# Performance work log

Measured on AMD Instinct MI355X. Metric: run time of the kernel, lower is better.

Reference implementation:

```python
import jax, jax.numpy as jnp
import numpy as np

B, L, IN_DIM, OUT_DIM = 4, 2048, 64, 2
D_MODEL, N_LAYERS = 768, 4
D_STATE, EXPAND, D_CONV = 16, 2, 4
D_INNER = EXPAND * D_MODEL          # 1536
DT_RANK = -(-D_MODEL // 16)          # ceil(768/16) = 48
EPS = 1e-5


def rmsnorm(x, w):
    return x * jax.lax.rsqrt(jnp.mean(x * x, axis=-1, keepdims=True) + EPS) * w


def setup_inputs() -> dict:
    key = jax.random.key(0)
    ks = jax.random.split(key, 10)
    s = 0.02
    f = lambda k, shp: jax.random.normal(k, shp, jnp.float32) * s
    return dict(
        x=jax.random.normal(ks[0], (B, L, IN_DIM), jnp.float32),
        W1=f(ks[1], (D_MODEL, IN_DIM)),
        b1=jnp.zeros((D_MODEL,), jnp.float32),
        norm_w=jnp.ones((N_LAYERS, D_MODEL), jnp.float32),
        in_proj_w=f(ks[2], (N_LAYERS, 2 * D_INNER, D_MODEL)),
        conv_w=f(ks[3], (N_LAYERS, D_INNER, D_CONV)),
        conv_b=jnp.zeros((N_LAYERS, D_INNER), jnp.float32),
        x_proj_w=f(ks[4], (N_LAYERS, DT_RANK + 2 * D_STATE, D_INNER)),
        dt_proj_w=f(ks[5], (N_LAYERS, D_INNER, DT_RANK)),
        dt_proj_b=f(ks[6], (N_LAYERS, D_INNER)),
        A_log=jnp.log(jnp.broadcast_to(jnp.arange(1, D_STATE + 1, dtype=jnp.float32), (N_LAYERS, D_INNER, D_STATE))).copy(),
        D=jnp.ones((N_LAYERS, D_INNER), jnp.float32),
        out_proj_w=f(ks[7], (N_LAYERS, D_MODEL, D_INNER)),
        normf_w=jnp.ones((D_MODEL,), jnp.float32),
        W2=f(ks[8], (OUT_DIM, D_MODEL)),
        b2=jnp.zeros((OUT_DIM,), jnp.float32),
    )


def _block(h, p):
    # One Mamba residual block (mamba-minimal): h + out_proj(ssm(conv(in_proj(norm(h)))))
    norm_w, in_w, cw, cb, xp_w, dt_w, dt_b, A_log, Dp, out_w = p
    xn = rmsnorm(h, norm_w)
    xr = xn @ in_w.T                                  # [B,L,2*d_inner]
    xs, res = jnp.split(xr, 2, axis=-1)
    # causal depthwise conv1d, kernel D_CONV, left pad D_CONV-1
    xc = jax.lax.conv_general_dilated(
        xs.transpose(0, 2, 1), cw[:, None, :], (1,), [(D_CONV - 1, 0)],
        feature_group_count=D_INNER, dimension_numbers=('NCH', 'OIH', 'NCH'))
    xc = jax.nn.silu((xc + cb[None, :, None]).transpose(0, 2, 1))  # [B,L,d_inner]
    # selective SSM
    A = -jnp.exp(A_log)                               # [d_inner, n]
    dbl = xc @ xp_w.T                                 # [B,L,dt_rank+2n]
    dr = dbl[..., :DT_RANK]
    Bm = dbl[..., DT_RANK:DT_RANK + D_STATE]          # [B,L,n]
    Cm = dbl[..., DT_RANK + D_STATE:]                 # [B,L,n]
    delta = jax.nn.softplus(dr @ dt_w.T + dt_b)       # [B,L,d_inner]

    def step(s, t):
        d_t, B_t, C_t, u_t = t                        # [B,d_in],[B,n],[B,n],[B,d_in]
        dA = jnp.exp(d_t[..., None] * A)              # [B,d_in,n]
        s = dA * s + (d_t * u_t)[..., None] * B_t[:, None, :]
        y = jnp.einsum('bdn,bn->bd', s, C_t)
        return s, y

    init = jnp.zeros((h.shape[0], D_INNER, D_STATE), h.dtype)
    ts = (delta.transpose(1, 0, 2), Bm.transpose(1, 0, 2),
          Cm.transpose(1, 0, 2), xc.transpose(1, 0, 2))
    _, ys = jax.lax.scan(step, init, ts)
    y = ys.transpose(1, 0, 2) + xc * Dp               # [B,L,d_inner]
    y = y * jax.nn.silu(res)
    return h + y @ out_w.T


def _forward(x, W1, b1, norm_w, in_proj_w, conv_w, conv_b, x_proj_w,
             dt_proj_w, dt_proj_b, A_log, D, out_proj_w, normf_w, W2, b2):
    h = x @ W1.T + b1                                 # [B,L,d_model]
    params = (norm_w, in_proj_w, conv_w, conv_b, x_proj_w, dt_proj_w,
              dt_proj_b, A_log, D, out_proj_w)
    h, _ = jax.lax.scan(lambda c, p: (_block(c, p), None), h, params)
    h = rmsnorm(h, normf_w)
    logits = h @ W2.T + b2                            # [B,L,out_dim]
    probs = jax.nn.softmax(logits, axis=1)            # Softmax(dim=1) over L
    return probs.reshape(-1)                          # x.flatten()


def reference(x, W1, b1, norm_w, in_proj_w, conv_w, conv_b, x_proj_w,
              dt_proj_w, dt_proj_b, A_log, D, out_proj_w, normf_w, W2, b2):
    return _forward(x, W1, b1, norm_w, in_proj_w, conv_w, conv_b, x_proj_w,
                    dt_proj_w, dt_proj_b, A_log, D, out_proj_w, normf_w, W2, b2)
```

## Files before the change

kernel.cpp:

```cpp
#include <hip/hip_runtime.h>

typedef __bf16 bf16_t;
typedef bf16_t bf16x8 __attribute__((ext_vector_type(8)));
typedef float f32x4 __attribute__((ext_vector_type(4)));
typedef float f32x2 __attribute__((ext_vector_type(2)));

#define DEV_INLINE __device__ __forceinline__

#define BB 4
#define LL 2048
#define ROWS 8192
#define DMODEL 768
#define DINNER 1536
#define DIN2 3072
#define DTRANK 48
#define DSTATE 16

DEV_INLINE void glds16(const void* g, void* l) {
    __builtin_amdgcn_global_load_lds(
        (const __attribute__((address_space(1))) void*)(unsigned long long)g,
        (__attribute__((address_space(3))) void*)(unsigned int)(unsigned long long)l,
        16, 0, 0);
}

DEV_INLINE float bf2f(bf16_t v) { return (float)v; }
DEV_INLINE bf16_t f2bf(float v) { return (bf16_t)v; }

struct Ptrs { const void* p[16]; };

__device__ __constant__ const int g_off[16] = {
    0, 524288, 573440, 574208, 577280, 10014464, 10039040, 10045184,
    10536704, 10831616, 10837760, 10936064, 10942208, 15660800, 15661568, 15663104
};
__device__ __constant__ const int g_sz[16] = {
    524288, 49152, 768, 3072, 9437184, 24576, 6144, 491520,
    294912, 6144, 98304, 6144, 4718592, 768, 1536, 2
};
#define CONV_ELEMS 15663112

__global__ __launch_bounds__(256) void convert_inputs(Ptrs P, bf16_t* __restrict__ dst,
                                                      float* __restrict__ Aa)
{
    int gi = (blockIdx.x * 256 + threadIdx.x) * 8;
    if (gi >= CONV_ELEMS) return;
    bool isbf = (*(const unsigned*)P.p[3] == 0x3F803F80u);
    int seg = -1, rel = 0;
#pragma unroll
    for (int s = 0; s < 16; ++s) {
        int r = gi - g_off[s];
        if (r >= 0 && r < g_sz[s]) { seg = s; rel = r; }
    }
    if (seg >= 0 && rel + 8 <= g_sz[seg]) {
        const void* sp = P.p[seg];
        float f[8];
        if (isbf) {
            bf16x8 v = *(const bf16x8*)((const bf16_t*)sp + rel);
#pragma unroll
            for (int k = 0; k < 8; ++k) f[k] = bf2f(v[k]);
        } else {
            f32x4 v0 = *(const f32x4*)((const float*)sp + rel);
            f32x4 v1 = *(const f32x4*)((const float*)sp + rel + 4);
#pragma unroll
            for (int k = 0; k < 4; ++k) { f[k] = v0[k]; f[k + 4] = v1[k]; }
        }
        bf16x8 o;
#pragma unroll
        for (int k = 0; k < 8; ++k) o[k] = f2bf(f[k]);
        *(bf16x8*)(dst + gi) = o;
        if (seg == 10) {
#pragma unroll
            for (int k = 0; k < 8; ++k) Aa[rel + k] = -__expf(f[k]);
        }
    } else {
        for (int k = 0; k < 8; ++k) {
            int i = gi + k;
            int s2 = -1, r2 = 0;
#pragma unroll
            for (int s = 0; s < 16; ++s) {
                int r = i - g_off[s];
                if (r >= 0 && r < g_sz[s]) { s2 = s; r2 = r; }
            }
            if (s2 < 0) continue;
            const void* sp = P.p[s2];
            float fv = isbf ? bf2f(((const bf16_t*)sp)[r2]) : ((const float*)sp)[r2];
            dst[i] = f2bf(fv);
            if (s2 == 10) Aa[r2] = -__expf(fv);
        }
    }
}

__global__ __launch_bounds__(256) void gemm_bt128(
    const bf16_t* __restrict__ A, int lda,
    const bf16_t* __restrict__ W, int ldw,
    void* __restrict__ Cv, int ldc, int K,
    const bf16_t* __restrict__ bias, int epi)
{
    __shared__ bf16_t sA[2][128 * 32];
    __shared__ bf16_t sW[2][128 * 32];
    const int t = threadIdx.x;
    const int wv = t >> 6, lane = t & 63;
    const int qk = lane >> 4, lr = lane & 15;
    const int m0 = blockIdx.x * 128, n0 = blockIdx.y * 128;
    const int wm = (wv >> 1) * 64, wn = (wv & 1) * 64;

    int ch0 = (wv * 2 + 0) * 64 + lane;
    int ch1 = (wv * 2 + 1) * 64 + lane;
    int r0 = ch0 >> 2, g0 = (ch0 & 3) ^ ((r0 >> 1) & 3);
    int r1 = ch1 >> 2, g1 = (ch1 & 3) ^ ((r1 >> 1) & 3);

    f32x4 acc[4][4];
#pragma unroll
    for (int i = 0; i < 4; ++i)
#pragma unroll
        for (int j = 0; j < 4; ++j) acc[i][j] = (f32x4){0.f, 0.f, 0.f, 0.f};

    {
        glds16((const char*)(A + (size_t)(m0 + r0) * lda) + g0 * 16, (char*)sA[0] + ch0 * 16);
        glds16((const char*)(A + (size_t)(m0 + r1) * lda) + g1 * 16, (char*)sA[0] + ch1 * 16);
        glds16((const char*)(W + (size_t)(n0 + r0) * ldw) + g0 * 16, (char*)sW[0] + ch0 * 16);
        glds16((const char*)(W + (size_t)(n0 + r1) * ldw) + g1 * 16, (char*)sW[0] + ch1 * 16);
    }

    int nIter = K >> 5;
    for (int it = 0; it < nIter; ++it) {
        int cur = it & 1;
        __syncthreads();
        if (it + 1 < nIter) {
            int k1 = (it + 1) << 5;
            glds16((const char*)(A + (size_t)(m0 + r0) * lda + k1) + g0 * 16,
                   (char*)sA[1 - cur] + ch0 * 16);
            glds16((const char*)(A + (size_t)(m0 + r1) * lda + k1) + g1 * 16,
                   (char*)sA[1 - cur] + ch1 * 16);
            glds16((const char*)(W + (size_t)(n0 + r0) * ldw + k1) + g0 * 16,
                   (char*)sW[1 - cur] + ch0 * 16);
            glds16((const char*)(W + (size_t)(n0 + r1) * ldw + k1) + g1 * 16,
                   (char*)sW[1 - cur] + ch1 * 16);
        }

        bf16x8 af[4], wf[4];
#pragma unroll
        for (int i = 0; i < 4; ++i) {
            int row = wm + i * 16 + lr;
            int cc = qk ^ ((row >> 1) & 3);
            af[i] = *(const bf16x8*)((const char*)sA[cur] + row * 64 + cc * 16);
        }
#pragma unroll
        for (int j = 0; j < 4; ++j) {
            int row = wn + j * 16 + lr;
            int cc = qk ^ ((row >> 1) & 3);
            wf[j] = *(const bf16x8*)((const char*)sW[cur] + row * 64 + cc * 16);
        }
#pragma unroll
        for (int i = 0; i < 4; ++i)
#pragma unroll
            for (int j = 0; j < 4; ++j)
                acc[i][j] = __builtin_amdgcn_mfma_f32_16x16x32_bf16(af[i], wf[j], acc[i][j], 0, 0, 0);
    }

    float* Cf = (float*)Cv;
    bf16_t* Cb = (bf16_t*)Cv;
#pragma unroll
    for (int i = 0; i < 4; ++i) {
        int row = m0 + wm + i * 16 + qk * 4;
#pragma unroll
        for (int j = 0; j < 4; ++j) {
            int col = n0 + wn + j * 16 + lr;
#pragma unroll
            for (int r = 0; r < 4; ++r) {
                size_t idx = (size_t)(row + r) * ldc + col;
                float v = acc[i][j][r];
                if (epi == 1) v += bf2f(bias[col]);
                if (epi == 2) v += Cf[idx];
                if (epi == 3) Cb[idx] = f2bf(v);
                else Cf[idx] = v;
            }
        }
    }
}

__global__ __launch_bounds__(256) void gemm_outproj(
    const bf16_t* __restrict__ A,
    const bf16_t* __restrict__ W,
    float* __restrict__ Cf)
{
    __shared__ bf16_t sA[2][64 * 32];
    __shared__ bf16_t sW[2][128 * 32];
    const int t = threadIdx.x;
    const int wv = t >> 6, lane = t & 63;
    const int qk = lane >> 4, lr = lane & 15;
    const int m0 = blockIdx.x * 64, n0 = blockIdx.y * 128;
    const int wm = (wv >> 1) * 32, wn = (wv & 1) * 64;

    int ca = wv * 64 + lane;
    int ra = ca >> 2, ga = (ca & 3) ^ ((ra >> 1) & 3);
    int cw0 = (wv * 2 + 0) * 64 + lane;
    int cw1 = (wv * 2 + 1) * 64 + lane;
    int rw0 = cw0 >> 2, gw0 = (cw0 & 3) ^ ((rw0 >> 1) & 3);
    int rw1 = cw1 >> 2, gw1 = (cw1 & 3) ^ ((rw1 >> 1) & 3);

    f32x2 accv[4];
    (void)accv;

    f32x4 acc[2][4];
#pragma unroll
    for (int i = 0; i < 2; ++i)
#pragma unroll
        for (int j = 0; j < 4; ++j) acc[i][j] = (f32x4){0.f, 0.f, 0.f, 0.f};

    {
        glds16((const char*)(A + (size_t)(m0 + ra) * DINNER) + ga * 16, (char*)sA[0] + ca * 16);
        glds16((const char*)(W + (size_t)(n0 + rw0) * DINNER) + gw0 * 16, (char*)sW[0] + cw0 * 16);
        glds16((const char*)(W + (size_t)(n0 + rw1) * DINNER) + gw1 * 16, (char*)sW[0] + cw1 * 16);
    }

    const int nIter = DINNER / 32;
    for (int it = 0; it < nIter; ++it) {
        int cur = it & 1;
        __syncthreads();
        if (it + 1 < nIter) {
            int k1 = (it + 1) << 5;
            glds16((const char*)(A + (size_t)(m0 + ra) * DINNER + k1) + ga * 16,
                   (char*)sA[1 - cur] + ca * 16);
            glds16((const char*)(W + (size_t)(n0 + rw0) * DINNER + k1) + gw0 * 16,
                   (char*)sW[1 - cur] + cw0 * 16);
            glds16((const char*)(W + (size_t)(n0 + rw1) * DINNER + k1) + gw1 * 16,
                   (char*)sW[1 - cur] + cw1 * 16);
        }

        bf16x8 af[2], wf[4];
#pragma unroll
        for (int i = 0; i < 2; ++i) {
            int row = wm + i * 16 + lr;
            int cc = qk ^ ((row >> 1) & 3);
            af[i] = *(const bf16x8*)((const char*)sA[cur] + row * 64 + cc * 16);
        }
#pragma unroll
        for (int j = 0; j < 4; ++j) {
            int row = wn + j * 16 + lr;
            int cc = qk ^ ((row >> 1) & 3);
            wf[j] = *(const bf16x8*)((const char*)sW[cur] + row * 64 + cc * 16);
        }
#pragma unroll
        for (int i = 0; i < 2; ++i)
#pragma unroll
            for (int j = 0; j < 4; ++j)
                acc[i][j] = __builtin_amdgcn_mfma_f32_16x16x32_bf16(af[i], wf[j], acc[i][j], 0, 0, 0);
    }

#pragma unroll
    for (int i = 0; i < 2; ++i) {
        int row = m0 + wm + i * 16 + qk * 4;
#pragma unroll
        for (int j = 0; j < 4; ++j) {
            int col = n0 + wn + j * 16 + lr;
#pragma unroll
            for (int r = 0; r < 4; ++r) {
                size_t idx = (size_t)(row + r) * DMODEL + col;
                Cf[idx] += acc[i][j][r];
            }
        }
    }
}

__global__ __launch_bounds__(256) void gemm_xproj(
    const bf16_t* __restrict__ A,
    const bf16_t* __restrict__ W,
    float* __restrict__ Cp)
{
    __shared__ bf16_t sA[64 * 32];
    __shared__ bf16_t sW[80 * 32];
    const int t = threadIdx.x;
    const int wv = t >> 6, lane = t & 63;
    const int qk = lane >> 4, lr = lane & 15;
    const int m0 = blockIdx.x * 64;
    const int z  = blockIdx.y;
    const int wm = wv * 16;

    f32x4 acc[5];
#pragma unroll
    for (int j = 0; j < 5; ++j) acc[j] = (f32x4){0.f, 0.f, 0.f, 0.f};

    const int kbeg = z * (DINNER / 2), kend = kbeg + DINNER / 2;
    for (int k0 = kbeg; k0 < kend; k0 += 32) {
        __syncthreads();
        {
            int chunk = wv * 64 + lane;
            int row = chunk >> 2;
            int c = chunk & 3;
            int g = c ^ ((row >> 1) & 3);
            const char* srcA = (const char*)(A + (size_t)(m0 + row) * DINNER + k0) + g * 16;
            glds16(srcA, (char*)sA + wv * 1024);
        }
        for (int issue = wv; issue < 5; issue += 4) {
            int chunk = issue * 64 + lane;
            int row = chunk >> 2;
            int c = chunk & 3;
            int g = c ^ ((row >> 1) & 3);
            const char* srcW = (const char*)(W + (size_t)row * DINNER + k0) + g * 16;
            glds16(srcW, (char*)sW + issue * 1024);
        }
        __syncthreads();

        int rowa = wm + lr;
        int cca = qk ^ ((rowa >> 1) & 3);
        bf16x8 af = *(const bf16x8*)((const char*)sA + rowa * 64 + cca * 16);
#pragma unroll
        for (int j = 0; j < 5; ++j) {
            int roww = j * 16 + lr;
            int ccw = qk ^ ((roww >> 1) & 3);
            bf16x8 wf = *(const bf16x8*)((const char*)sW + roww * 64 + ccw * 16);
            acc[j] = __builtin_amdgcn_mfma_f32_16x16x32_bf16(af, wf, acc[j], 0, 0, 0);
        }
    }

    float* Co = Cp + (size_t)z * ROWS * 80;
    int row = m0 + wm + qk * 4;
#pragma unroll
    for (int j = 0; j < 5; ++j) {
        int col = j * 16 + lr;
#pragma unroll
        for (int r = 0; r < 4; ++r)
            Co[(size_t)(row + r) * 80 + col] = acc[j][r];
    }
}

__global__ __launch_bounds__(256) void xproj_combine(
    const float* __restrict__ Cp, bf16_t* __restrict__ dbl)
{
    int i = blockIdx.x * 256 + threadIdx.x;
    if (i < ROWS * 80)
        dbl[i] = f2bf(Cp[i] + Cp[(size_t)ROWS * 80 + i]);
}

__global__ __launch_bounds__(256) void gemm_dtproj(
    const bf16_t* __restrict__ A,
    const bf16_t* __restrict__ W,
    const bf16_t* __restrict__ bias,
    bf16_t* __restrict__ C)
{
    __shared__ bf16_t sA[128 * 64];
    __shared__ bf16_t sW[128 * 64];
    const int t = threadIdx.x;
    const int wv = t >> 6, lane = t & 63;
    const int qk = lane >> 4, lr = lane & 15;
    const int m0 = blockIdx.x * 128, n0 = blockIdx.y * 128;
    const int wm = (wv >> 1) * 64, wn = (wv & 1) * 64;

#pragma unroll
    for (int j = 0; j < 4; ++j) {
        int ci = j * 256 + t;
        int row = ci >> 3;
        int g = (ci & 7) ^ (row & 7);
        int gb = g * 16;
        uint4 va = {0u, 0u, 0u, 0u}, vw = {0u, 0u, 0u, 0u};
        if (gb < 96) {
            va = *(const uint4*)((const char*)(A + (size_t)(m0 + row) * 80) + gb);
            vw = *(const uint4*)((const char*)(W + (size_t)(n0 + row) * DTRANK) + gb);
        }
        *(uint4*)((char*)sA + ci * 16) = va;
        *(uint4*)((char*)sW + ci * 16) = vw;
    }
    __syncthreads();

    f32x4 acc[4][4];
#pragma unroll
    for (int i = 0; i < 4; ++i)
#pragma unroll
        for (int j = 0; j < 4; ++j) acc[i][j] = (f32x4){0.f, 0.f, 0.f, 0.f};

#pragma unroll
    for (int h = 0; h < 2; ++h) {
        bf16x8 af[4], wf[4];
#pragma unroll
        for (int i = 0; i < 4; ++i) {
            int row = wm + i * 16 + lr;
            int cc = (h * 4 + qk) ^ (row & 7);
            af[i] = *(const bf16x8*)((const char*)sA + row * 128 + cc * 16);
        }
#pragma unroll
        for (int j = 0; j < 4; ++j) {
            int row = wn + j * 16 + lr;
            int cc = (h * 4 + qk) ^ (row & 7);
            wf[j] = *(const bf16x8*)((const char*)sW + row * 128 + cc * 16);
        }
#pragma unroll
        for (int i = 0; i < 4; ++i)
#pragma unroll
            for (int j = 0; j < 4; ++j)
                acc[i][j] = __builtin_amdgcn_mfma_f32_16x16x32_bf16(af[i], wf[j], acc[i][j], 0, 0, 0);
    }

#pragma unroll
    for (int i = 0; i < 4; ++i) {
        int row = m0 + wm + i * 16 + qk * 4;
#pragma unroll
        for (int j = 0; j < 4; ++j) {
            int col = n0 + wn + j * 16 + lr;
            float bv = bf2f(bias[col]);
#pragma unroll
            for (int r = 0; r < 4; ++r) {
                float v = acc[i][j][r] + bv;
                v = (v > 30.f) ? v : log1pf(__expf(v));
                C[(size_t)(row + r) * DINNER + col] = f2bf(v);
            }
        }
    }
}

__global__ __launch_bounds__(256) void rmsnorm_kernel(
    const float* __restrict__ h, const bf16_t* __restrict__ w, bf16_t* __restrict__ out)
{
    int row = blockIdx.x;
    int tid = threadIdx.x;
    const float* hr = h + (size_t)row * DMODEL;
    float ss = 0.f;
    for (int k = tid; k < DMODEL; k += 256) { float v = hr[k]; ss += v * v; }
#pragma unroll
    for (int off = 32; off > 0; off >>= 1) ss += __shfl_down(ss, off);
    __shared__ float red[4];
    if ((tid & 63) == 0) red[tid >> 6] = ss;
    __syncthreads();
    float tot = red[0] + red[1] + red[2] + red[3];
    float scale = rsqrtf(tot / (float)DMODEL + 1e-5f);
    for (int k = tid; k < DMODEL; k += 256)
        out[(size_t)row * DMODEL + k] = f2bf(hr[k] * scale * bf2f(w[k]));
}

__global__ __launch_bounds__(256) void conv_silu_kernel(
    const bf16_t* __restrict__ xr, const bf16_t* __restrict__ cw,
    const bf16_t* __restrict__ cb, bf16_t* __restrict__ xc)
{
    int idx = blockIdx.x * 256 + threadIdx.x;
    int row = idx / 192;
    int d8 = (idx - row * 192) * 8;
    int l = row & (LL - 1);

    bf16x8 cbv = *(const bf16x8*)(cb + d8);
    bf16x8 cw4[4];
#pragma unroll
    for (int m = 0; m < 4; ++m) cw4[m] = *(const bf16x8*)(cw + d8 * 4 + m * 8);

    float acc[8];
#pragma unroll
    for (int k = 0; k < 8; ++k) acc[k] = bf2f(cbv[k]);

#pragma unroll
    for (int j = 0; j < 4; ++j) {
        if (l - 3 + j >= 0) {
            bf16x8 xv = *(const bf16x8*)(xr + (size_t)(row - 3 + j) * DIN2 + d8);
#pragma unroll
            for (int k = 0; k < 8; ++k) {
                int wi = k * 4 + j;
                acc[k] += bf2f(xv[k]) * bf2f(cw4[wi >> 3][wi & 7]);
            }
        }
    }
    bf16x8 ov;
#pragma unroll
    for (int k = 0; k < 8; ++k) {
        float s = acc[k] / (1.f + __expf(-acc[k]));
        ov[k] = f2bf(s);
    }
    *(bf16x8*)(xc + (size_t)row * DINNER + d8) = ov;
}

DEV_INLINE f32x2 pk2(float a, float b) { f32x2 v; v[0] = a; v[1] = b; return v; }

__global__ __launch_bounds__(256) void scan_p1(
    const bf16_t* __restrict__ delta, const bf16_t* __restrict__ xc,
    const bf16_t* __restrict__ dbl, const float* __restrict__ Aa_l,
    float* __restrict__ carryDt, float* __restrict__ carryE,
    int nchunk, int clen)
{
    int d = blockIdx.x * 256 + threadIdx.x;
    int b = blockIdx.y / nchunk, c = blockIdx.y - b * nchunk;
    float Aa[DSTATE];
#pragma unroll
    for (int n = 0; n < DSTATE; ++n) Aa[n] = Aa_l[d * DSTATE + n];
    float Aa0 = Aa[0];
    bool geo = true;
#pragma unroll
    for (int n = 1; n < DSTATE; ++n)
        geo = geo && (fabsf(Aa[n] - (float)(n + 1) * Aa0) <= 0.02f * (float)(n + 1) * fabsf(Aa0));

    f32x2 s2[8];
#pragma unroll
    for (int k = 0; k < 8; ++k) s2[k] = pk2(0.f, 0.f);
    float dtsum = 0.f;
    int row0 = b * LL + c * clen;

    if (geo) {
        for (int tt = 0; tt < clen; ++tt) {
            size_t row = row0 + tt;
            float dt = bf2f(delta[row * DINNER + d]);
            float du = dt * bf2f(xc[row * DINNER + d]);
            bf16x8 B0 = *(const bf16x8*)(dbl + row * 80 + 48);
            bf16x8 B1 = *(const bf16x8*)(dbl + row * 80 + 56);
            float r = __expf(dt * Aa0);
            float rr = r * r;
            f32x2 rr2 = pk2(rr, rr);
            f32x2 dA = pk2(r, rr);
            f32x2 du2 = pk2(du, du);
#pragma unroll
            for (int k = 0; k < 8; ++k) {
                f32x2 bv = (k < 4) ? pk2(bf2f(B0[2 * k]), bf2f(B0[2 * k + 1]))
                                   : pk2(bf2f(B1[2 * k - 8]), bf2f(B1[2 * k - 7]));
                s2[k] = dA * s2[k] + du2 * bv;
                dA *= rr2;
            }
            dtsum += dt;
        }
    } else {
        for (int tt = 0; tt < clen; ++tt) {
            size_t row = row0 + tt;
            float dt = bf2f(delta[row * DINNER + d]);
            float du = dt * bf2f(xc[row * DINNER + d]);
            bf16x8 B0 = *(const bf16x8*)(dbl + row * 80 + 48);
            bf16x8 B1 = *(const bf16x8*)(dbl + row * 80 + 56);
            f32x2 du2 = pk2(du, du);
#pragma unroll
            for (int k = 0; k < 8; ++k) {
                f32x2 bv = (k < 4) ? pk2(bf2f(B0[2 * k]), bf2f(B0[2 * k + 1]))
                                   : pk2(bf2f(B1[2 * k - 8]), bf2f(B1[2 * k - 7]));
                f32x2 e = pk2(__expf(dt * Aa[2 * k]), __expf(dt * Aa[2 * k + 1]));
                s2[k] = e * s2[k] + du2 * bv;
            }
            dtsum += dt;
        }
    }

    size_t eb = ((size_t)(b * nchunk + c) * DINNER + d) * DSTATE;
#pragma unroll
    for (int k = 0; k < 8; ++k) {
        carryE[eb + 2 * k] = s2[k][0];
        carryE[eb + 2 * k + 1] = s2[k][1];
    }
    carryDt[(size_t)(b * nchunk + c) * DINNER + d] = dtsum;
}

__global__ __launch_bounds__(256) void scan_p2(
    const float* __restrict__ carryDt, float* __restrict__ carryE,
    const float* __restrict__ Aa_l, int nchunk)
{
    int idx = blockIdx.x * 256 + threadIdx.x;
    int n = idx & 15;
    int bd = idx >> 4;
    int b = bd / DINNER, d = bd - b * DINNER;
    float Aa = Aa_l[d * DSTATE + n];
    float act = 0.f;
    for (int c = 0; c < nchunk; ++c) {
        size_t rowbase = (size_t)(b * nchunk + c) * DINNER + d;
        float P = __expf(carryDt[rowbase] * Aa);
        size_t ep = rowbase * DSTATE + n;
        float E = carryE[ep];
        carryE[ep] = act;
        act = P * act + E;
    }
}

__global__ __launch_bounds__(256) void scan_p3(
    const bf16_t* __restrict__ delta, const bf16_t* __restrict__ xc,
    const bf16_t* __restrict__ dbl, const float* __restrict__ Aa_l,
    const float* __restrict__ carryInit, const bf16_t* __restrict__ xr,
    const bf16_t* __restrict__ Dp_l, bf16_t* __restrict__ y,
    int nchunk, int clen)
{
    int d = blockIdx.x * 256 + threadIdx.x;
    int b = blockIdx.y / nchunk, c = blockIdx.y - b * nchunk;
    float Aa[DSTATE];
#pragma unroll
    for (int n = 0; n < DSTATE; ++n) Aa[n] = Aa_l[d * DSTATE + n];
    float Aa0 = Aa[0];
    bool geo = true;
#pragma unroll
    for (int n = 1; n < DSTATE; ++n)
        geo = geo && (fabsf(Aa[n] - (float)(n + 1) * Aa0) <= 0.02f * (float)(n + 1) * fabsf(Aa0));

    f32x2 s2[8];
    size_t eb = ((size_t)(b * nchunk + c) * DINNER + d) * DSTATE;
#pragma unroll
    for (int k = 0; k < 8; ++k)
        s2[k] = pk2(carryInit[eb + 2 * k], carryInit[eb + 2 * k + 1]);
    float Dv = bf2f(Dp_l[d]);
    int row0 = b * LL + c * clen;

    if (geo) {
        for (int tt = 0; tt < clen; ++tt) {
            size_t row = row0 + tt;
            float dt = bf2f(delta[row * DINNER + d]);
            float u = bf2f(xc[row * DINNER + d]);
            float du = dt * u;
            bf16x8 B0 = *(const bf16x8*)(dbl + row * 80 + 48);
            bf16x8 B1 = *(const bf16x8*)(dbl + row * 80 + 56);
            bf16x8 C0 = *(const bf16x8*)(dbl + row * 80 + 64);
            bf16x8 C1 = *(const bf16x8*)(dbl + row * 80 + 72);
            float r = __expf(dt * Aa0);
            float rr = r * r;
            f32x2 rr2 = pk2(rr, rr);
            f32x2 dA = pk2(r, rr);
            f32x2 du2 = pk2(du, du);
            f32x2 yv2 = pk2(0.f, 0.f);
#pragma unroll
            for (int k = 0; k < 8; ++k) {
                f32x2 bv = (k < 4) ? pk2(bf2f(B0[2 * k]), bf2f(B0[2 * k + 1]))
                                   : pk2(bf2f(B1[2 * k - 8]), bf2f(B1[2 * k - 7]));
                f32x2 cv = (k < 4) ? pk2(bf2f(C0[2 * k]), bf2f(C0[2 * k + 1]))
                                   : pk2(bf2f(C1[2 * k - 8]), bf2f(C1[2 * k - 7]));
                s2[k] = dA * s2[k] + du2 * bv;
                yv2 += s2[k] * cv;
                dA *= rr2;
            }
            float yv = yv2[0] + yv2[1];
            float res = bf2f(xr[row * DIN2 + DINNER + d]);
            float sr = res / (1.f + __expf(-res));
            y[row * DINNER + d] = f2bf((yv + u * Dv) * sr);
        }
    } else {
        for (int tt = 0; tt < clen; ++tt) {
            size_t row = row0 + tt;
            float dt = bf2f(delta[row * DINNER + d]);
            float u = bf2f(xc[row * DINNER + d]);
            float du = dt * u;
            bf16x8 B0 = *(const bf16x8*)(dbl + row * 80 + 48);
            bf16x8 B1 = *(const bf16x8*)(dbl + row * 80 + 56);
            bf16x8 C0 = *(const bf16x8*)(dbl + row * 80 + 64);
            bf16x8 C1 = *(const bf16x8*)(dbl + row * 80 + 72);
            f32x2 du2 = pk2(du, du);
            f32x2 yv2 = pk2(0.f, 0.f);
#pragma unroll
            for (int k = 0; k < 8; ++k) {
                f32x2 bv = (k < 4) ? pk2(bf2f(B0[2 * k]), bf2f(B0[2 * k + 1]))
                                   : pk2(bf2f(B1[2 * k - 8]), bf2f(B1[2 * k - 7]));
                f32x2 cv = (k < 4) ? pk2(bf2f(C0[2 * k]), bf2f(C0[2 * k + 1]))
                                   : pk2(bf2f(C1[2 * k - 8]), bf2f(C1[2 * k - 7]));
                f32x2 e = pk2(__expf(dt * Aa[2 * k]), __expf(dt * Aa[2 * k + 1]));
                s2[k] = e * s2[k] + du2 * bv;
                yv2 += s2[k] * cv;
            }
            float yv = yv2[0] + yv2[1];
            float res = bf2f(xr[row * DIN2 + DINNER + d]);
            float sr = res / (1.f + __expf(-res));
            y[row * DINNER + d] = f2bf((yv + u * Dv) * sr);
        }
    }
}

__global__ __launch_bounds__(256) void head_kernel(
    const bf16_t* __restrict__ hn, const bf16_t* __restrict__ W2,
    const bf16_t* __restrict__ b2, float* __restrict__ logits)
{
    int wv = threadIdx.x >> 6, lane = threadIdx.x & 63;
    int row = blockIdx.x * 4 + wv;
    const bf16_t* hr = hn + (size_t)row * DMODEL;
    float a0 = 0.f, a1 = 0.f;
    for (int k = lane; k < DMODEL; k += 64) {
        float x = bf2f(hr[k]);
        a0 += x * bf2f(W2[k]);
        a1 += x * bf2f(W2[DMODEL + k]);
    }
#pragma unroll
    for (int off = 32; off > 0; off >>= 1) {
        a0 += __shfl_down(a0, off);
        a1 += __shfl_down(a1, off);
    }
    if (lane == 0) {
        logits[(size_t)row * 2 + 0] = a0 + bf2f(b2[0]);
        logits[(size_t)row * 2 + 1] = a1 + bf2f(b2[1]);
    }
}

__global__ __launch_bounds__(256) void softmax_kernel(
    const float* __restrict__ logits, void* __restrict__ outv,
    const void* __restrict__ norm_raw)
{
    bool isbf = (*(const unsigned*)norm_raw == 0x3F803F80u);
    int b = blockIdx.x >> 1, o = blockIdx.x & 1;
    int tid = threadIdx.x;
    __shared__ float red[256];
    float mx = -1e30f;
    for (int l = tid; l < LL; l += 256)
        mx = fmaxf(mx, logits[(size_t)(b * LL + l) * 2 + o]);
    red[tid] = mx; __syncthreads();
    for (int s2 = 128; s2 > 0; s2 >>= 1) {
        if (tid < s2) red[tid] = fmaxf(red[tid], red[tid + s2]);
        __syncthreads();
    }
    mx = red[0];
    __syncthreads();
    float sum = 0.f;
    for (int l = tid; l < LL; l += 256)
        sum += __expf(logits[(size_t)(b * LL + l) * 2 + o] - mx);
    red[tid] = sum; __syncthreads();
    for (int s2 = 128; s2 > 0; s2 >>= 1) {
        if (tid < s2) red[tid] += red[tid + s2];
        __syncthreads();
    }
    float inv = 1.f / red[0];
    for (int l = tid; l < LL; l += 256) {
        float e = __expf(logits[(size_t)(b * LL + l) * 2 + o] - mx);
        float p = e * inv;
        if (!(p == p)) p = 999.0f;
        size_t oi = (size_t)(b * LL + l) * 2 + o;
        if (isbf) ((bf16_t*)outv)[oi] = f2bf(p);
        else      ((float*)outv)[oi] = p;
    }
}

extern "C" void kernel_launch(void* const* d_in, const int* in_sizes, int n_in,
                              void* d_out, int out_size, void* d_ws, size_t ws_size,
                              hipStream_t stream)
{
    char* ws = (char*)d_ws;
    bf16_t* cv     = (bf16_t*)(ws + 0ull);
    float*  Aaf    = (float*) (ws + 31326464ull);
    float*  h      = (float*) (ws + 31719680ull);
    bf16_t* xr     = (bf16_t*)(ws + 56885504ull);
    bf16_t* xny    = (bf16_t*)(ws + 107217152ull);
    bf16_t* xc     = (bf16_t*)(ws + 132382976ull);
    bf16_t* delta  = (bf16_t*)(ws + 157548800ull);
    bf16_t* dbl    = (bf16_t*)(ws + 182714624ull);
    float*  logits = (float*) (ws + 184025344ull);
    const size_t fixed_end = 184090880ull;
    float* dblP = (float*)(ws + 157548800ull);

    int nchunk = 16;
    if (ws_size >= fixed_end + 417792ull * 64) nchunk = 64;
    else if (ws_size >= fixed_end + 417792ull * 32) nchunk = 32;
    int clen = LL / nchunk;
    float* carryE  = (float*)(ws + fixed_end);
    float* carryDt = (float*)(ws + fixed_end + 393216ull * nchunk);

    const bf16_t* x      = cv + 0;
    const bf16_t* W1     = cv + 524288;
    const bf16_t* b1     = cv + 573440;
    const bf16_t* norm_w = cv + 574208;
    const bf16_t* in_w   = cv + 577280;
    const bf16_t* conv_w = cv + 10014464;
    const bf16_t* conv_b = cv + 10039040;
    const bf16_t* xp_w   = cv + 10045184;
    const bf16_t* dt_w   = cv + 10536704;
    const bf16_t* dt_b   = cv + 10831616;
    const bf16_t* Dp     = cv + 10936064;
    const bf16_t* out_w  = cv + 10942208;
    const bf16_t* normf_w= cv + 15660800;
    const bf16_t* W2     = cv + 15661568;
    const bf16_t* b2     = cv + 15663104;

    dim3 blk(256);

    Ptrs P;
    for (int i = 0; i < 16; ++i) P.p[i] = d_in[i];
    convert_inputs<<<(CONV_ELEMS / 8 + 255) / 256, blk, 0, stream>>>(P, cv, Aaf);

    bf16_t* xn = xny;
    bf16_t* y  = xny;

    gemm_bt128<<<dim3(64, 6), blk, 0, stream>>>(x, 64, W1, 64, (void*)h, DMODEL, 64, b1, 1);

    for (int l = 0; l < 4; ++l) {
        const bf16_t* in_w_l  = in_w  + (size_t)l * DIN2 * DMODEL;
        const bf16_t* xp_w_l  = xp_w  + (size_t)l * 80 * DINNER;
        const bf16_t* dt_w_l  = dt_w  + (size_t)l * DINNER * DTRANK;
        const bf16_t* out_w_l = out_w + (size_t)l * DMODEL * DINNER;
        const float*  Aa_l    = Aaf   + (size_t)l * DINNER * DSTATE;

        rmsnorm_kernel<<<ROWS, blk, 0, stream>>>(h, norm_w + l * DMODEL, xn);
        gemm_bt128<<<dim3(64, 24), blk, 0, stream>>>(xn, DMODEL, in_w_l, DMODEL,
                                                     (void*)xr, DIN2, DMODEL, nullptr, 3);
        conv_silu_kernel<<<ROWS * 192 / 256, blk, 0, stream>>>(xr, conv_w + l * DINNER * 4,
                                                               conv_b + l * DINNER, xc);
        gemm_xproj<<<dim3(128, 2), blk, 0, stream>>>(xc, xp_w_l, dblP);
        xproj_combine<<<ROWS * 80 / 256, blk, 0, stream>>>(dblP, dbl);
        gemm_dtproj<<<dim3(64, 12), blk, 0, stream>>>(dbl, dt_w_l, dt_b + l * DINNER, delta);
        scan_p1<<<dim3(6, BB * nchunk), blk, 0, stream>>>(delta, xc, dbl, Aa_l,
                                                          carryDt, carryE, nchunk, clen);
        scan_p2<<<BB * DINNER * DSTATE / 256, blk, 0, stream>>>(carryDt, carryE, Aa_l, nchunk);
        scan_p3<<<dim3(6, BB * nchunk), blk, 0, stream>>>(delta, xc, dbl, Aa_l, carryE,
                                                          xr, Dp + l * DINNER, y, nchunk, clen);
        gemm_outproj<<<dim3(128, 6), blk, 0, stream>>>(y, out_w_l, h);
    }

    rmsnorm_kernel<<<ROWS, blk, 0, stream>>>(h, normf_w, xn);
    head_kernel<<<ROWS / 4, blk, 0, stream>>>(xn, W2, b2, logits);
    softmax_kernel<<<8, blk, 0, stream>>>(logits, (void*)d_out, d_in[3]);
}
```

Measured before the change: 1.244 ms.

## Fuse conv+SiLU into x_proj GEMM, split-K combine into dt_proj, norm into head

The depthwise causal conv and SiLU now run inside the x_proj GEMM's A-tile load. The result is written both to shared memory and to global xc, so the separate conv kernel and its xc re-read go away. The split-K partial-sum combine moves into dt_proj's prologue: block column 0 also writes the B/C columns of dbl, and the standalone combine kernel is removed. The final RMSNorm is fused with the output head into a single per-row warp kernel. In exchange, the GEMM prologue now does scalar conv math per K-step with synchronous loads instead of async global-to-LDS copies, and the fp32 partials buffer is moved to alias the xn/y buffer.

```diff
diff --git a/kernel.cpp b/kernel.cpp
--- a/kernel.cpp
+++ b/kernel.cpp
@@ -198,9 +198,6 @@
     int rw0 = cw0 >> 2, gw0 = (cw0 & 3) ^ ((rw0 >> 1) & 3);
     int rw1 = cw1 >> 2, gw1 = (cw1 & 3) ^ ((rw1 >> 1) & 3);
 
-    f32x2 accv[4];
-    (void)accv;
-
     f32x4 acc[2][4];
 #pragma unroll
     for (int i = 0; i < 2; ++i)
@@ -262,10 +259,10 @@
     }
 }
 
-__global__ __launch_bounds__(256) void gemm_xproj(
-    const bf16_t* __restrict__ A,
-    const bf16_t* __restrict__ W,
-    float* __restrict__ Cp)
+__global__ __launch_bounds__(256) void gemm_xproj_conv(
+    const bf16_t* __restrict__ xr, const bf16_t* __restrict__ cw,
+    const bf16_t* __restrict__ cb, const bf16_t* __restrict__ W,
+    float* __restrict__ Cp, bf16_t* __restrict__ xc)
 {
     __shared__ bf16_t sA[64 * 32];
     __shared__ bf16_t sW[80 * 32];
@@ -276,6 +273,11 @@
     const int z  = blockIdx.y;
     const int wm = wv * 16;
 
+    const int row_l = t >> 2;
+    const int dd    = t & 3;
+    const int grow  = m0 + row_l;
+    const int l     = grow & (LL - 1);
+
     f32x4 acc[5];
 #pragma unroll
     for (int j = 0; j < 5; ++j) acc[j] = (f32x4){0.f, 0.f, 0.f, 0.f};
@@ -284,12 +286,34 @@
     for (int k0 = kbeg; k0 < kend; k0 += 32) {
         __syncthreads();
         {
-            int chunk = wv * 64 + lane;
-            int row = chunk >> 2;
-            int c = chunk & 3;
-            int g = c ^ ((row >> 1) & 3);
-            const char* srcA = (const char*)(A + (size_t)(m0 + row) * DINNER + k0) + g * 16;
-            glds16(srcA, (char*)sA + wv * 1024);
+            int d = k0 + dd * 8;
+            bf16x8 cbv = *(const bf16x8*)(cb + d);
+            bf16x8 cw4[4];
+#pragma unroll
+            for (int m = 0; m < 4; ++m) cw4[m] = *(const bf16x8*)(cw + d * 4 + m * 8);
+            float a8[8];
+#pragma unroll
+            for (int k = 0; k < 8; ++k) a8[k] = bf2f(cbv[k]);
+#pragma unroll
+            for (int j = 0; j < 4; ++j) {
+                if (l - 3 + j >= 0) {
+                    bf16x8 xv = *(const bf16x8*)(xr + (size_t)(grow - 3 + j) * DIN2 + d);
+#pragma unroll
+                    for (int k = 0; k < 8; ++k) {
+                        int wi = k * 4 + j;
+                        a8[k] += bf2f(xv[k]) * bf2f(cw4[wi >> 3][wi & 7]);
+                    }
+                }
+            }
+            bf16x8 val;
+#pragma unroll
+            for (int k = 0; k < 8; ++k) {
+                float s = a8[k] / (1.f + __expf(-a8[k]));
+                val[k] = f2bf(s);
+            }
+            int cc = dd ^ ((row_l >> 1) & 3);
+            *(bf16x8*)((char*)sA + row_l * 64 + cc * 16) = val;
+            *(bf16x8*)(xc + (size_t)grow * DINNER + d) = val;
         }
         for (int issue = wv; issue < 5; issue += 4) {
             int chunk = issue * 64 + lane;
@@ -324,19 +348,12 @@
     }
 }
 
-__global__ __launch_bounds__(256) void xproj_combine(
-    const float* __restrict__ Cp, bf16_t* __restrict__ dbl)
-{
-    int i = blockIdx.x * 256 + threadIdx.x;
-    if (i < ROWS * 80)
-        dbl[i] = f2bf(Cp[i] + Cp[(size_t)ROWS * 80 + i]);
-}
-
 __global__ __launch_bounds__(256) void gemm_dtproj(
-    const bf16_t* __restrict__ A,
+    const float* __restrict__ Cp,
     const bf16_t* __restrict__ W,
     const bf16_t* __restrict__ bias,
-    bf16_t* __restrict__ C)
+    bf16_t* __restrict__ C,
+    bf16_t* __restrict__ dbl)
 {
     __shared__ bf16_t sA[128 * 64];
     __shared__ bf16_t sW[128 * 64];
@@ -345,20 +362,53 @@
     const int qk = lane >> 4, lr = lane & 15;
     const int m0 = blockIdx.x * 128, n0 = blockIdx.y * 128;
     const int wm = (wv >> 1) * 64, wn = (wv & 1) * 64;
+    const float* Cp0 = Cp;
+    const float* Cp1 = Cp + (size_t)ROWS * 80;
 
 #pragma unroll
     for (int j = 0; j < 4; ++j) {
         int ci = j * 256 + t;
         int row = ci >> 3;
         int g = (ci & 7) ^ (row & 7);
-        int gb = g * 16;
-        uint4 va = {0u, 0u, 0u, 0u}, vw = {0u, 0u, 0u, 0u};
-        if (gb < 96) {
-            va = *(const uint4*)((const char*)(A + (size_t)(m0 + row) * 80) + gb);
-            vw = *(const uint4*)((const char*)(W + (size_t)(n0 + row) * DTRANK) + gb);
-        }
-        *(uint4*)((char*)sA + ci * 16) = va;
+        int e0 = g * 8;
+        bf16x8 av = {};
+        if (e0 < 48) {
+            size_t base = (size_t)(m0 + row) * 80 + e0;
+            f32x4 a0 = *(const f32x4*)(Cp0 + base);
+            f32x4 a1 = *(const f32x4*)(Cp0 + base + 4);
+            f32x4 b0 = *(const f32x4*)(Cp1 + base);
+            f32x4 b1 = *(const f32x4*)(Cp1 + base + 4);
+#pragma unroll
+            for (int k = 0; k < 4; ++k) {
+                av[k] = f2bf(a0[k] + b0[k]);
+                av[k + 4] = f2bf(a1[k] + b1[k]);
+            }
+        }
+        *(bf16x8*)((char*)sA + ci * 16) = av;
+        uint4 vw = {0u, 0u, 0u, 0u};
+        if (e0 < 48)
+            vw = *(const uint4*)((const char*)(W + (size_t)(n0 + row) * DTRANK) + e0 * 2);
         *(uint4*)((char*)sW + ci * 16) = vw;
+    }
+    if (blockIdx.y == 0) {
+#pragma unroll
+        for (int k = 0; k < 2; ++k) {
+            int oc = k * 256 + t;
+            int row = oc >> 2;
+            int cs = 48 + (oc & 3) * 8;
+            size_t base = (size_t)(m0 + row) * 80 + cs;
+            f32x4 a0 = *(const f32x4*)(Cp0 + base);
+            f32x4 a1 = *(const f32x4*)(Cp0 + base + 4);
+            f32x4 b0 = *(const f32x4*)(Cp1 + base);
+            f32x4 b1 = *(const f32x4*)(Cp1 + base + 4);
+            bf16x8 ov;
+#pragma unroll
+            for (int q = 0; q < 4; ++q) {
+                ov[q] = f2bf(a0[q] + b0[q]);
+                ov[q + 4] = f2bf(a1[q] + b1[q]);
+            }
+            *(bf16x8*)(dbl + base) = ov;
+        }
     }
     __syncthreads();
 
@@ -426,42 +476,38 @@
         out[(size_t)row * DMODEL + k] = f2bf(hr[k] * scale * bf2f(w[k]));
 }
 
-__global__ __launch_bounds__(256) void conv_silu_kernel(
-    const bf16_t* __restrict__ xr, const bf16_t* __restrict__ cw,
-    const bf16_t* __restrict__ cb, bf16_t* __restrict__ xc)
-{
-    int idx = blockIdx.x * 256 + threadIdx.x;
-    int row = idx / 192;
-    int d8 = (idx - row * 192) * 8;
-    int l = row & (LL - 1);
-
-    bf16x8 cbv = *(const bf16x8*)(cb + d8);
-    bf16x8 cw4[4];
-#pragma unroll
-    for (int m = 0; m < 4; ++m) cw4[m] = *(const bf16x8*)(cw + d8 * 4 + m * 8);
-
-    float acc[8];
-#pragma unroll
-    for (int k = 0; k < 8; ++k) acc[k] = bf2f(cbv[k]);
-
-#pragma unroll
-    for (int j = 0; j < 4; ++j) {
-        if (l - 3 + j >= 0) {
-            bf16x8 xv = *(const bf16x8*)(xr + (size_t)(row - 3 + j) * DIN2 + d8);
-#pragma unroll
-            for (int k = 0; k < 8; ++k) {
-                int wi = k * 4 + j;
-                acc[k] += bf2f(xv[k]) * bf2f(cw4[wi >> 3][wi & 7]);
-            }
-        }
-    }
-    bf16x8 ov;
-#pragma unroll
-    for (int k = 0; k < 8; ++k) {
-        float s = acc[k] / (1.f + __expf(-acc[k]));
-        ov[k] = f2bf(s);
-    }
-    *(bf16x8*)(xc + (size_t)row * DINNER + d8) = ov;
+__global__ __launch_bounds__(256) void rmsnorm_head(
+    const float* __restrict__ h, const bf16_t* __restrict__ w,
+    const bf16_t* __restrict__ W2, const bf16_t* __restrict__ b2,
+    float* __restrict__ logits)
+{
+    int wv = threadIdx.x >> 6, lane = threadIdx.x & 63;
+    int row = blockIdx.x * 4 + wv;
+    const float* hr = h + (size_t)row * DMODEL;
+    float v[12];
+    float ss = 0.f;
+#pragma unroll
+    for (int i = 0; i < 12; ++i) { v[i] = hr[lane + i * 64]; ss += v[i] * v[i]; }
+#pragma unroll
+    for (int off = 32; off > 0; off >>= 1) ss += __shfl_xor(ss, off);
+    float scale = rsqrtf(ss / (float)DMODEL + 1e-5f);
+    float a0 = 0.f, a1 = 0.f;
+#pragma unroll
+    for (int i = 0; i < 12; ++i) {
+        int k = lane + i * 64;
+        float xn = v[i] * scale * bf2f(w[k]);
+        a0 += xn * bf2f(W2[k]);
+        a1 += xn * bf2f(W2[DMODEL + k]);
+    }
+#pragma unroll
+    for (int off = 32; off > 0; off >>= 1) {
+        a0 += __shfl_xor(a0, off);
+        a1 += __shfl_xor(a1, off);
+    }
+    if (lane == 0) {
+        logits[(size_t)row * 2 + 0] = a0 + bf2f(b2[0]);
+        logits[(size_t)row * 2 + 1] = a1 + bf2f(b2[1]);
+    }
 }
 
 DEV_INLINE f32x2 pk2(float a, float b) { f32x2 v; v[0] = a; v[1] = b; return v; }
@@ -645,30 +691,6 @@
     }
 }
 
-__global__ __launch_bounds__(256) void head_kernel(
-    const bf16_t* __restrict__ hn, const bf16_t* __restrict__ W2,
-    const bf16_t* __restrict__ b2, float* __restrict__ logits)
-{
-    int wv = threadIdx.x >> 6, lane = threadIdx.x & 63;
-    int row = blockIdx.x * 4 + wv;
-    const bf16_t* hr = hn + (size_t)row * DMODEL;
-    float a0 = 0.f, a1 = 0.f;
-    for (int k = lane; k < DMODEL; k += 64) {
-        float x = bf2f(hr[k]);
-        a0 += x * bf2f(W2[k]);
-        a1 += x * bf2f(W2[DMODEL + k]);
-    }
-#pragma unroll
-    for (int off = 32; off > 0; off >>= 1) {
-        a0 += __shfl_down(a0, off);
-        a1 += __shfl_down(a1, off);
-    }
-    if (lane == 0) {
-        logits[(size_t)row * 2 + 0] = a0 + bf2f(b2[0]);
-        logits[(size_t)row * 2 + 1] = a1 + bf2f(b2[1]);
-    }
-}
-
 __global__ __launch_bounds__(256) void softmax_kernel(
     const float* __restrict__ logits, void* __restrict__ outv,
     const void* __restrict__ norm_raw)
@@ -721,7 +743,7 @@
     bf16_t* dbl    = (bf16_t*)(ws + 182714624ull);
     float*  logits = (float*) (ws + 184025344ull);
     const size_t fixed_end = 184090880ull;
-    float* dblP = (float*)(ws + 157548800ull);
+    float* dblP = (float*)xny;
 
     int nchunk = 16;
     if (ws_size >= fixed_end + 417792ull * 64) nchunk = 64;
@@ -767,11 +789,11 @@
         rmsnorm_kernel<<<ROWS, blk, 0, stream>>>(h, norm_w + l * DMODEL, xn);
         gemm_bt128<<<dim3(64, 24), blk, 0, stream>>>(xn, DMODEL, in_w_l, DMODEL,
                                                      (void*)xr, DIN2, DMODEL, nullptr, 3);
-        conv_silu_kernel<<<ROWS * 192 / 256, blk, 0, stream>>>(xr, conv_w + l * DINNER * 4,
-                                                               conv_b + l * DINNER, xc);
-        gemm_xproj<<<dim3(128, 2), blk, 0, stream>>>(xc, xp_w_l, dblP);
-        xproj_combine<<<ROWS * 80 / 256, blk, 0, stream>>>(dblP, dbl);
-        gemm_dtproj<<<dim3(64, 12), blk, 0, stream>>>(dbl, dt_w_l, dt_b + l * DINNER, delta);
+        gemm_xproj_conv<<<dim3(128, 2), blk, 0, stream>>>(xr, conv_w + l * DINNER * 4,
+                                                          conv_b + l * DINNER, xp_w_l,
+                                                          dblP, xc);
+        gemm_dtproj<<<dim3(64, 12), blk, 0, stream>>>(dblP, dt_w_l, dt_b + l * DINNER,
+                                                      delta, dbl);
         scan_p1<<<dim3(6, BB * nchunk), blk, 0, stream>>>(delta, xc, dbl, Aa_l,
                                                           carryDt, carryE, nchunk, clen);
         scan_p2<<<BB * DINNER * DSTATE / 256, blk, 0, stream>>>(carryDt, carryE, Aa_l, nchunk);
@@ -780,7 +802,6 @@
         gemm_outproj<<<dim3(128, 6), blk, 0, stream>>>(y, out_w_l, h);
     }
 
-    rmsnorm_kernel<<<ROWS, blk, 0, stream>>>(h, normf_w, xn);
-    head_kernel<<<ROWS / 4, blk, 0, stream>>>(xn, W2, b2, logits);
+    rmsnorm_head<<<ROWS / 4, blk, 0, stream>>>(h, normf_w, W2, b2, logits);
     softmax_kernel<<<8, blk, 0, stream>>>(logits, (void*)d_out, d_in[3]);
 }
```

Result: no change. 1.264 ms (+1.6%).
